# Performance work log

Measured on AMD Instinct MI355X. Metric: run time of the kernel, lower is better.

## Reference

```python
import jax, jax.numpy as jnp
import numpy as np

N, C_IN, C_OUT, T, V, S = 128, 64, 64, 256, 25, 3
INTER = C_OUT // 4  # coff_embedding = 4
BN_EPS = 1e-5


def conv1x1(x, w, b):
    # x: (n, c, t, v), w: (o, c), b: (o,) -- 1x1 Conv2d over (T, V)
    return jnp.einsum('nctv,oc->notv', x, w) + b[None, :, None, None]


def setup_inputs() -> dict:
    key = jax.random.key(0)
    ks = jax.random.split(key, 12)
    x = jax.random.normal(ks[0], (N, C_IN, T, V), jnp.float32)
    # A: fixed (non-trainable) adjacency subsets; graph_attn: learned, init ~1
    A = jax.random.normal(ks[1], (S, V, V), jnp.float32) * 0.1
    graph_attn = jnp.ones((S, V, V), jnp.float32) + 0.01 * jax.random.normal(ks[2], (S, V, V), jnp.float32)
    sc_in = 1.0 / np.sqrt(C_IN).astype(np.float32)
    a_w = jax.random.normal(ks[3], (S, INTER, C_IN), jnp.float32) * sc_in
    a_b = jax.random.normal(ks[4], (S, INTER), jnp.float32) * 0.01
    b_w = jax.random.normal(ks[5], (S, INTER, C_IN), jnp.float32) * sc_in
    b_b = jax.random.normal(ks[6], (S, INTER), jnp.float32) * 0.01
    g_w = jax.random.normal(ks[7], (S, C_OUT, C_IN), jnp.float32) * (sc_in / S)  # branch-scaled init
    g_b = jax.random.normal(ks[8], (S, C_OUT), jnp.float32) * 0.01
    bn_gamma = jnp.ones((C_OUT,), jnp.float32)
    bn_beta = jnp.zeros((C_OUT,), jnp.float32)
    return {"x": x, "A": A, "graph_attn": graph_attn, "a_w": a_w, "a_b": a_b,
            "b_w": b_w, "b_b": b_b, "g_w": g_w, "g_b": g_b,
            "bn_gamma": bn_gamma, "bn_beta": bn_beta}


def reference(x, A, graph_attn, a_w, a_b, b_w, b_b, g_w, g_b, bn_gamma, bn_beta):
    Afull = A + graph_attn                       # (S, V, V)
    inter = a_w.shape[1]
    hidden = None
    for i in range(a_w.shape[0]):                # 3 structurally distinct subsets
        A1 = conv1x1(x, a_w[i], a_b[i]).transpose(0, 3, 1, 2)  # (n, v, c_inter, t)
        A2 = conv1x1(x, b_w[i], b_b[i])                        # (n, c_inter, t, w)
        scores = jnp.einsum('nvct,nctw->nvwt', A1, A2) / inter # (n, v, w, t)
        attn = jax.nn.softmax(scores, axis=-2)                 # softmax over w (dim -2)
        attn = attn + Afull[i][None, :, :, None]               # learned adjacency bias
        # NOTE: faithful to the source einsum: w is contracted, v is batched,
        # so z[n,c,t,v] = x[n,c,t,v] * sum_w attn[n,v,w,t]
        z = jnp.einsum('nctv,nvwt->nctv', x, attn)
        g = conv1x1(z, g_w[i], g_b[i])
        hidden = g if hidden is None else hidden + g
    # BatchNorm2d, training-mode batch statistics over (N, T, V), biased var
    mean = hidden.mean(axis=(0, 2, 3), keepdims=True)
    var = hidden.var(axis=(0, 2, 3), keepdims=True)
    h = (hidden - mean) * jax.lax.rsqrt(var + BN_EPS)
    h = h * bn_gamma[None, :, None, None] + bn_beta[None, :, None, None]
    # in_channels == out_channels -> identity residual
    return jax.nn.relu(h + x)
```

## Files before the change

### kernel.cpp

```cpp
#include <hip/hip_runtime.h>

#define NN 128
#define CC 64
#define TT 256
#define VV 25
#define NSUB 3
#define TCH 8
#define LPOS (TCH*VV)
#define NCHUNK (TT/TCH)
#define CNT (NN*TT*VV)
#define XSTR 204
#define WROW (VV*CC)

#define WS_BEFF 80
#define WS_GSUM 144
#define WS_GSQ  208
#define WS_W    320
#define WS_BFIN (WS_W + VV*CC*CC)

__global__ void k_weff(const float* __restrict__ A, const float* __restrict__ ga,
                       const float* __restrict__ gw, const float* __restrict__ gb,
                       float* __restrict__ ws) {
    __shared__ float S[NSUB*VV];
    int tid = threadIdx.x;
    if (tid < NSUB*VV) {
        int i = tid / VV, v = tid % VV;
        const float* pa = A  + (i*VV + v)*VV;
        const float* pg = ga + (i*VV + v)*VV;
        float s = 0.f;
        for (int w2 = 0; w2 < VV; ++w2) s += pa[w2] + pg[w2];
        S[tid] = s;
    }
    __syncthreads();
    int idx = blockIdx.x*256 + tid;
    int v = idx >> 12;
    int c = (idx >> 6) & 63;
    int o = idx & 63;
    float acc = 0.f;
    #pragma unroll
    for (int i = 0; i < NSUB; ++i)
        acc = fmaf(gw[(i*CC + o)*CC + c], 1.f + S[i*VV + v], acc);
    ws[WS_W + c*WROW + v*CC + o] = acc;
    if (blockIdx.x == 0 && tid < CC)
        ws[WS_BEFF + tid] = gb[tid] + gb[CC + tid] + gb[2*CC + tid];
    if (blockIdx.x == 1 && tid < 128)
        ws[WS_GSUM + tid] = 0.f;
}

__global__ __launch_bounds__(256, 3) void k_stats(const float* __restrict__ x,
                                                  const float* __restrict__ wsw,
                                                  float* __restrict__ gsum,
                                                  float* __restrict__ gsq) {
    __shared__ __align__(16) float Xs[CC*XSTR];
    __shared__ float s_sum[CC], s_sq[CC];
    int tid = threadIdx.x;
    int n = blockIdx.x >> 5, ch = blockIdx.x & 31;
    const float* xb = x + (size_t)n*(CC*TT*VV) + ch*LPOS;
    if (tid < CC) { s_sum[tid] = 0.f; s_sq[tid] = 0.f; }
    for (int i4 = tid; i4 < CC*(LPOS/4); i4 += 256) {
        int c = i4 / (LPOS/4), j4 = i4 - c*(LPOS/4);
        *(float4*)&Xs[c*XSTR + j4*4] = *(const float4*)(xb + c*(TT*VV) + j4*4);
    }
    __syncthreads();
    if (tid < 200) {
        int og = tid & 7, v = tid >> 3, o0 = og*8;
        float acc[TCH][8];
        #pragma unroll
        for (int t = 0; t < TCH; ++t)
            #pragma unroll
            for (int b = 0; b < 8; ++b) acc[t][b] = 0.f;
        const float* wp = wsw + v*CC + o0;
        const float* xp = Xs + v;
        #pragma unroll 4
        for (int c = 0; c < CC; ++c) {
            const float* wr = wp + c*WROW;
            float4 w0 = *(const float4*)(wr);
            float4 w1 = *(const float4*)(wr + 4);
            float xv[TCH];
            #pragma unroll
            for (int t = 0; t < TCH; ++t) xv[t] = xp[c*XSTR + t*VV];
            #pragma unroll
            for (int t = 0; t < TCH; ++t) {
                float xx = xv[t];
                acc[t][0] = fmaf(xx, w0.x, acc[t][0]);
                acc[t][1] = fmaf(xx, w0.y, acc[t][1]);
                acc[t][2] = fmaf(xx, w0.z, acc[t][2]);
                acc[t][3] = fmaf(xx, w0.w, acc[t][3]);
                acc[t][4] = fmaf(xx, w1.x, acc[t][4]);
                acc[t][5] = fmaf(xx, w1.y, acc[t][5]);
                acc[t][6] = fmaf(xx, w1.z, acc[t][6]);
                acc[t][7] = fmaf(xx, w1.w, acc[t][7]);
            }
        }
        #pragma unroll
        for (int oi = 0; oi < 8; ++oi) {
            float s1 = 0.f, s2 = 0.f;
            #pragma unroll
            for (int t = 0; t < TCH; ++t) {
                s1 += acc[t][oi];
                s2 = fmaf(acc[t][oi], acc[t][oi], s2);
            }
            atomicAdd(&s_sum[o0+oi], s1);
            atomicAdd(&s_sq[o0+oi],  s2);
        }
    }
    __syncthreads();
    if (tid < CC) {
        atomicAdd(&gsum[tid], s_sum[tid]);
        atomicAdd(&gsq[tid],  s_sq[tid]);
    }
}

__global__ void k_mid(float* __restrict__ ws, const float* __restrict__ gamma,
                      const float* __restrict__ beta) {
    int idx = blockIdx.x*256 + threadIdx.x;
    int o = idx & 63;
    int c = idx / WROW;
    float b     = ws[WS_BEFF + o];
    float meanY = ws[WS_GSUM + o] * (1.f/CNT);
    float ey2   = ws[WS_GSQ  + o] * (1.f/CNT);
    float m   = meanY + b;
    float var = ey2 + 2.f*b*meanY + b*b - m*m;
    float alpha = gamma[o] * rsqrtf(var + 1e-5f);
    float wv = ws[WS_W + idx];
    ws[WS_W + idx] = fmaf(alpha, wv, (c == o) ? 1.f : 0.f);
    if (blockIdx.x == 0 && threadIdx.x < CC)
        ws[WS_BFIN + o] = fmaf(alpha, b - m, beta[o]);
}

__global__ __launch_bounds__(256, 3) void k_final(const float* __restrict__ x,
                                                  const float* __restrict__ ws,
                                                  float* __restrict__ out) {
    __shared__ __align__(16) float Xs[CC*XSTR];
    int tid = threadIdx.x;
    int n = blockIdx.x >> 5, ch = blockIdx.x & 31;
    const float* xb = x + (size_t)n*(CC*TT*VV) + ch*LPOS;
    for (int i4 = tid; i4 < CC*(LPOS/4); i4 += 256) {
        int c = i4 / (LPOS/4), j4 = i4 - c*(LPOS/4);
        *(float4*)&Xs[c*XSTR + j4*4] = *(const float4*)(xb + c*(TT*VV) + j4*4);
    }
    __syncthreads();
    if (tid < 200) {
        int og = tid & 7, v = tid >> 3, o0 = og*8;
        float acc[TCH][8];
        #pragma unroll
        for (int t = 0; t < TCH; ++t)
            #pragma unroll
            for (int b = 0; b < 8; ++b) acc[t][b] = 0.f;
        const float* wp = ws + WS_W + v*CC + o0;
        const float* xp = Xs + v;
        #pragma unroll 4
        for (int c = 0; c < CC; ++c) {
            const float* wr = wp + c*WROW;
            float4 w0 = *(const float4*)(wr);
            float4 w1 = *(const float4*)(wr + 4);
            float xv[TCH];
            #pragma unroll
            for (int t = 0; t < TCH; ++t) xv[t] = xp[c*XSTR + t*VV];
            #pragma unroll
            for (int t = 0; t < TCH; ++t) {
                float xx = xv[t];
                acc[t][0] = fmaf(xx, w0.x, acc[t][0]);
                acc[t][1] = fmaf(xx, w0.y, acc[t][1]);
                acc[t][2] = fmaf(xx, w0.z, acc[t][2]);
                acc[t][3] = fmaf(xx, w0.w, acc[t][3]);
                acc[t][4] = fmaf(xx, w1.x, acc[t][4]);
                acc[t][5] = fmaf(xx, w1.y, acc[t][5]);
                acc[t][6] = fmaf(xx, w1.z, acc[t][6]);
                acc[t][7] = fmaf(xx, w1.w, acc[t][7]);
            }
        }
        #pragma unroll
        for (int oi = 0; oi < 8; ++oi) {
            float bfo = ws[WS_BFIN + o0 + oi];
            #pragma unroll
            for (int t = 0; t < TCH; ++t)
                Xs[(o0+oi)*XSTR + t*VV + v] = fmaxf(acc[t][oi] + bfo, 0.f);
        }
    }
    __syncthreads();
    float* ob = out + (size_t)n*(CC*TT*VV) + ch*LPOS;
    for (int i4 = tid; i4 < CC*(LPOS/4); i4 += 256) {
        int o = i4 / (LPOS/4), j4 = i4 - o*(LPOS/4);
        *(float4*)(ob + o*(TT*VV) + j4*4) = *(const float4*)&Xs[o*XSTR + j4*4];
    }
}

extern "C" void kernel_launch(void* const* d_in, const int* in_sizes, int n_in,
                              void* d_out, int out_size, void* d_ws, size_t ws_size,
                              hipStream_t stream) {
    const float* x     = (const float*)d_in[0];
    const float* A     = (const float*)d_in[1];
    const float* ga    = (const float*)d_in[2];
    const float* gw    = (const float*)d_in[7];
    const float* gb    = (const float*)d_in[8];
    const float* gamma = (const float*)d_in[9];
    const float* beta  = (const float*)d_in[10];
    float* ws  = (float*)d_ws;
    float* out = (float*)d_out;

    hipLaunchKernelGGL(k_weff,  dim3(400), dim3(256), 0, stream, A, ga, gw, gb, ws);
    hipLaunchKernelGGL(k_stats, dim3(NN*NCHUNK), dim3(256), 0, stream,
                       x, ws + WS_W, ws + WS_GSUM, ws + WS_GSQ);
    hipLaunchKernelGGL(k_mid,   dim3(400), dim3(256), 0, stream, ws, gamma, beta);
    hipLaunchKernelGGL(k_final, dim3(NN*NCHUNK), dim3(256), 0, stream, x, ws, out);
}
```

Before: 647.0 us.

## Materialize GEMM output once instead of recomputing it after BN stats

Replaces the two-pass scheme, which ran the full channel-mixing GEMM twice (once for batch statistics, once for the final output), with a single GEMM pass that writes the pre-norm result to the output buffer while accumulating statistics. A small kernel then computes per-channel scale and shift, and an elementwise kernel applies the BN affine, the residual and the ReLU in place. This removes one full GEMM pass but adds an extra write and read of the output-sized tensor. The bias terms are dropped because training-mode BN cancels them. The variance now comes from E[y^2]-mean^2 on the raw GEMM output.

New measurement: 662.2 us. 2.4% more time.

```diff
diff --git a/kernel.cpp b/kernel.cpp
--- a/kernel.cpp
+++ b/kernel.cpp
@@ -12,15 +12,14 @@
 #define XSTR 204
 #define WROW (VV*CC)
 
-#define WS_BEFF 80
+#define WS_ALPHA 80
 #define WS_GSUM 144
 #define WS_GSQ  208
 #define WS_W    320
 #define WS_BFIN (WS_W + VV*CC*CC)
 
 __global__ void k_weff(const float* __restrict__ A, const float* __restrict__ ga,
-                       const float* __restrict__ gw, const float* __restrict__ gb,
-                       float* __restrict__ ws) {
+                       const float* __restrict__ gw, float* __restrict__ ws) {
     __shared__ float S[NSUB*VV];
     int tid = threadIdx.x;
     if (tid < NSUB*VV) {
@@ -41,100 +40,21 @@
     for (int i = 0; i < NSUB; ++i)
         acc = fmaf(gw[(i*CC + o)*CC + c], 1.f + S[i*VV + v], acc);
     ws[WS_W + c*WROW + v*CC + o] = acc;
-    if (blockIdx.x == 0 && tid < CC)
-        ws[WS_BEFF + tid] = gb[tid] + gb[CC + tid] + gb[2*CC + tid];
     if (blockIdx.x == 1 && tid < 128)
         ws[WS_GSUM + tid] = 0.f;
 }
 
-__global__ __launch_bounds__(256, 3) void k_stats(const float* __restrict__ x,
-                                                  const float* __restrict__ wsw,
-                                                  float* __restrict__ gsum,
-                                                  float* __restrict__ gsq) {
+__global__ __launch_bounds__(256, 3) void k_gemm(const float* __restrict__ x,
+                                                 const float* __restrict__ ws,
+                                                 float* __restrict__ y,
+                                                 float* __restrict__ gsum,
+                                                 float* __restrict__ gsq) {
     __shared__ __align__(16) float Xs[CC*XSTR];
     __shared__ float s_sum[CC], s_sq[CC];
     int tid = threadIdx.x;
     int n = blockIdx.x >> 5, ch = blockIdx.x & 31;
     const float* xb = x + (size_t)n*(CC*TT*VV) + ch*LPOS;
     if (tid < CC) { s_sum[tid] = 0.f; s_sq[tid] = 0.f; }
-    for (int i4 = tid; i4 < CC*(LPOS/4); i4 += 256) {
-        int c = i4 / (LPOS/4), j4 = i4 - c*(LPOS/4);
-        *(float4*)&Xs[c*XSTR + j4*4] = *(const float4*)(xb + c*(TT*VV) + j4*4);
-    }
-    __syncthreads();
-    if (tid < 200) {
-        int og = tid & 7, v = tid >> 3, o0 = og*8;
-        float acc[TCH][8];
-        #pragma unroll
-        for (int t = 0; t < TCH; ++t)
-            #pragma unroll
-            for (int b = 0; b < 8; ++b) acc[t][b] = 0.f;
-        const float* wp = wsw + v*CC + o0;
-        const float* xp = Xs + v;
-        #pragma unroll 4
-        for (int c = 0; c < CC; ++c) {
-            const float* wr = wp + c*WROW;
-            float4 w0 = *(const float4*)(wr);
-            float4 w1 = *(const float4*)(wr + 4);
-            float xv[TCH];
-            #pragma unroll
-            for (int t = 0; t < TCH; ++t) xv[t] = xp[c*XSTR + t*VV];
-            #pragma unroll
-            for (int t = 0; t < TCH; ++t) {
-                float xx = xv[t];
-                acc[t][0] = fmaf(xx, w0.x, acc[t][0]);
-                acc[t][1] = fmaf(xx, w0.y, acc[t][1]);
-                acc[t][2] = fmaf(xx, w0.z, acc[t][2]);
-                acc[t][3] = fmaf(xx, w0.w, acc[t][3]);
-                acc[t][4] = fmaf(xx, w1.x, acc[t][4]);
-                acc[t][5] = fmaf(xx, w1.y, acc[t][5]);
-                acc[t][6] = fmaf(xx, w1.z, acc[t][6]);
-                acc[t][7] = fmaf(xx, w1.w, acc[t][7]);
-            }
-        }
-        #pragma unroll
-        for (int oi = 0; oi < 8; ++oi) {
-            float s1 = 0.f, s2 = 0.f;
-            #pragma unroll
-            for (int t = 0; t < TCH; ++t) {
-                s1 += acc[t][oi];
-                s2 = fmaf(acc[t][oi], acc[t][oi], s2);
-            }
-            atomicAdd(&s_sum[o0+oi], s1);
-            atomicAdd(&s_sq[o0+oi],  s2);
-        }
-    }
-    __syncthreads();
-    if (tid < CC) {
-        atomicAdd(&gsum[tid], s_sum[tid]);
-        atomicAdd(&gsq[tid],  s_sq[tid]);
-    }
-}
-
-__global__ void k_mid(float* __restrict__ ws, const float* __restrict__ gamma,
-                      const float* __restrict__ beta) {
-    int idx = blockIdx.x*256 + threadIdx.x;
-    int o = idx & 63;
-    int c = idx / WROW;
-    float b     = ws[WS_BEFF + o];
-    float meanY = ws[WS_GSUM + o] * (1.f/CNT);
-    float ey2   = ws[WS_GSQ  + o] * (1.f/CNT);
-    float m   = meanY + b;
-    float var = ey2 + 2.f*b*meanY + b*b - m*m;
-    float alpha = gamma[o] * rsqrtf(var + 1e-5f);
-    float wv = ws[WS_W + idx];
-    ws[WS_W + idx] = fmaf(alpha, wv, (c == o) ? 1.f : 0.f);
-    if (blockIdx.x == 0 && threadIdx.x < CC)
-        ws[WS_BFIN + o] = fmaf(alpha, b - m, beta[o]);
-}
-
-__global__ __launch_bounds__(256, 3) void k_final(const float* __restrict__ x,
-                                                  const float* __restrict__ ws,
-                                                  float* __restrict__ out) {
-    __shared__ __align__(16) float Xs[CC*XSTR];
-    int tid = threadIdx.x;
-    int n = blockIdx.x >> 5, ch = blockIdx.x & 31;
-    const float* xb = x + (size_t)n*(CC*TT*VV) + ch*LPOS;
     for (int i4 = tid; i4 < CC*(LPOS/4); i4 += 256) {
         int c = i4 / (LPOS/4), j4 = i4 - c*(LPOS/4);
         *(float4*)&Xs[c*XSTR + j4*4] = *(const float4*)(xb + c*(TT*VV) + j4*4);
@@ -172,17 +92,62 @@
         }
         #pragma unroll
         for (int oi = 0; oi < 8; ++oi) {
-            float bfo = ws[WS_BFIN + o0 + oi];
+            float s1 = 0.f, s2 = 0.f;
+            #pragma unroll
+            for (int t = 0; t < TCH; ++t) {
+                s1 += acc[t][oi];
+                s2 = fmaf(acc[t][oi], acc[t][oi], s2);
+            }
+            atomicAdd(&s_sum[o0+oi], s1);
+            atomicAdd(&s_sq[o0+oi],  s2);
+        }
+        #pragma unroll
+        for (int oi = 0; oi < 8; ++oi) {
             #pragma unroll
             for (int t = 0; t < TCH; ++t)
-                Xs[(o0+oi)*XSTR + t*VV + v] = fmaxf(acc[t][oi] + bfo, 0.f);
+                Xs[(o0+oi)*XSTR + t*VV + v] = acc[t][oi];
         }
     }
     __syncthreads();
-    float* ob = out + (size_t)n*(CC*TT*VV) + ch*LPOS;
+    float* ob = y + (size_t)n*(CC*TT*VV) + ch*LPOS;
     for (int i4 = tid; i4 < CC*(LPOS/4); i4 += 256) {
         int o = i4 / (LPOS/4), j4 = i4 - o*(LPOS/4);
         *(float4*)(ob + o*(TT*VV) + j4*4) = *(const float4*)&Xs[o*XSTR + j4*4];
+    }
+    if (tid < CC) {
+        atomicAdd(&gsum[tid], s_sum[tid]);
+        atomicAdd(&gsq[tid],  s_sq[tid]);
+    }
+}
+
+__global__ void k_mid(float* __restrict__ ws, const float* __restrict__ gamma,
+                      const float* __restrict__ beta) {
+    int o = threadIdx.x;
+    float meanY = ws[WS_GSUM + o] * (1.f/CNT);
+    float ey2   = ws[WS_GSQ  + o] * (1.f/CNT);
+    float var   = ey2 - meanY*meanY;
+    float alpha = gamma[o] * rsqrtf(var + 1e-5f);
+    ws[WS_ALPHA + o] = alpha;
+    ws[WS_BFIN  + o] = fmaf(-alpha, meanY, beta[o]);
+}
+
+__global__ __launch_bounds__(256) void k_fin(const float* __restrict__ x,
+                                             float* __restrict__ y,
+                                             const float* __restrict__ ws) {
+    int o = blockIdx.x & 63;
+    float a = ws[WS_ALPHA + o];
+    float b = ws[WS_BFIN  + o];
+    size_t base = (size_t)blockIdx.x * (TT*VV);
+    const float4* xp = (const float4*)(x + base);
+    float4*       yp = (float4*)(y + base);
+    for (int j = threadIdx.x; j < (TT*VV)/4; j += 256) {
+        float4 yv = yp[j];
+        float4 xv = xp[j];
+        yv.x = fmaxf(fmaf(a, yv.x, b) + xv.x, 0.f);
+        yv.y = fmaxf(fmaf(a, yv.y, b) + xv.y, 0.f);
+        yv.z = fmaxf(fmaf(a, yv.z, b) + xv.z, 0.f);
+        yv.w = fmaxf(fmaf(a, yv.w, b) + xv.w, 0.f);
+        yp[j] = yv;
     }
 }
 
@@ -193,15 +158,14 @@
     const float* A     = (const float*)d_in[1];
     const float* ga    = (const float*)d_in[2];
     const float* gw    = (const float*)d_in[7];
-    const float* gb    = (const float*)d_in[8];
     const float* gamma = (const float*)d_in[9];
     const float* beta  = (const float*)d_in[10];
     float* ws  = (float*)d_ws;
     float* out = (float*)d_out;
 
-    hipLaunchKernelGGL(k_weff,  dim3(400), dim3(256), 0, stream, A, ga, gw, gb, ws);
-    hipLaunchKernelGGL(k_stats, dim3(NN*NCHUNK), dim3(256), 0, stream,
-                       x, ws + WS_W, ws + WS_GSUM, ws + WS_GSQ);
-    hipLaunchKernelGGL(k_mid,   dim3(400), dim3(256), 0, stream, ws, gamma, beta);
-    hipLaunchKernelGGL(k_final, dim3(NN*NCHUNK), dim3(256), 0, stream, x, ws, out);
+    hipLaunchKernelGGL(k_weff, dim3(400), dim3(256), 0, stream, A, ga, gw, ws);
+    hipLaunchKernelGGL(k_gemm, dim3(NN*NCHUNK), dim3(256), 0, stream,
+                       x, ws, out, ws + WS_GSUM, ws + WS_GSQ);
+    hipLaunchKernelGGL(k_mid,  dim3(1), dim3(64), 0, stream, ws, gamma, beta);
+    hipLaunchKernelGGL(k_fin,  dim3(NN*CC), dim3(256), 0, stream, x, out, ws);
 }
```
